# Kernel tuning notes

Measured on AMD Instinct MI355X. Metric: run time of the kernel, lower is better.

## Reference

```python
import jax, jax.numpy as jnp
import numpy as np

H = 512  # hidden size
E = 512  # embedding / input size
V = 10000  # vocab size


def _lstm_cell(x, h, c, W_ih, W_hh, b_ih, b_hh):
    # torch LSTMCell gate order: i, f, g, o
    gates = x @ W_ih.T + h @ W_hh.T + b_ih + b_hh
    i, f, g, o = jnp.split(gates, 4, axis=-1)
    i = jax.nn.sigmoid(i)
    f = jax.nn.sigmoid(f)
    g = jnp.tanh(g)
    o = jax.nn.sigmoid(o)
    c_new = f * c + i * g
    h_new = o * jnp.tanh(c_new)
    return h_new, c_new


def setup_inputs() -> dict:
    key = jax.random.key(0)
    ks = jax.random.split(key, 14)
    T, B, U = 128, 32, 1024
    s = 0.05
    return {
        "inputs": jax.random.normal(ks[0], (T, B, E), jnp.float32),
        "h0": jax.random.normal(ks[1], (2, B, H), jnp.float32),
        "c0": jax.random.normal(ks[2], (2, B, H), jnp.float32),
        "listener_outputs": jax.random.normal(ks[3], (U, B, H), jnp.float32),
        "W_ih1": jax.random.normal(ks[4], (4 * H, E), jnp.float32) * s,
        "W_hh1": jax.random.normal(ks[5], (4 * H, H), jnp.float32) * s,
        "b_ih1": jax.random.normal(ks[6], (4 * H,), jnp.float32) * s,
        "b_hh1": jax.random.normal(ks[7], (4 * H,), jnp.float32) * s,
        "W_ih2": jax.random.normal(ks[8], (4 * H, H), jnp.float32) * s,
        "W_hh2": jax.random.normal(ks[9], (4 * H, H), jnp.float32) * s,
        "b_ih2": jax.random.normal(ks[10], (4 * H,), jnp.float32) * s,
        "b_hh2": jax.random.normal(ks[11], (4 * H,), jnp.float32) * s,
        "W_out": jax.random.normal(ks[12], (V, H), jnp.float32) * s,
        "b_out": jax.random.normal(ks[13], (V,), jnp.float32) * s,
    }


def reference(inputs, h0, c0, listener_outputs,
              W_ih1, W_hh1, b_ih1, b_hh1,
              W_ih2, W_hh2, b_ih2, b_hh2,
              W_out, b_out):
    # layer-1 LSTMCell + dot-product attention per timestep
    def step1(carry, x_t):
        h1, c1 = carry
        h1, c1 = _lstm_cell(x_t, h1, c1, W_ih1, W_hh1, b_ih1, b_hh1)
        # scores over listener time U: (B, U)
        scores = jnp.einsum('ubh,bh->bu', listener_outputs, h1)
        w = jax.nn.softmax(scores, axis=1)
        ctx = jnp.einsum('ubh,bu->bh', listener_outputs, w)  # (B, H)
        return (h1, c1), ctx

    (_, _), contexts = jax.lax.scan(step1, (h0[0], c0[0]), inputs)  # (T, B, H)

    # layer-2 single-layer LSTM over attention contexts
    def step2(carry, x_t):
        h2, c2 = carry
        h2, c2 = _lstm_cell(x_t, h2, c2, W_ih2, W_hh2, b_ih2, b_hh2)
        return (h2, c2), h2

    (_, _), hs = jax.lax.scan(step2, (h0[1], c0[1]), contexts)  # (T, B, H)

    logits = hs @ W_out.T + b_out  # (T, B, V)
    return jax.nn.softmax(logits, axis=2)
```

## Files before the change

kernel.cpp:

```cpp
#include <hip/hip_runtime.h>

#define T_STEPS 128
#define BATCH   32
#define HID     512
#define EMB     512
#define ULEN    1024
#define VOCAB   10000
#define G4H     2048

#define ARR_STRIDE 16
#define GO_OFF     4096
#define GO_STRIDE  64
#define BAR_WORDS  6144

static inline int cdiv(int a, int b) { return (a + b - 1) / b; }

template <bool TRANSB>
__global__ __launch_bounds__(256)
void gemm_f32(const float* __restrict__ A, long lda, long sA,
              const float* __restrict__ Bm, long ldb, long sB,
              float* __restrict__ C, long ldc, long sC,
              int M, int N, int K, const float* __restrict__ bias)
{
    __shared__ float As[16][68];
    __shared__ float Bs[16][68];
    const int bz = blockIdx.z;
    A  += (size_t)bz * sA;
    Bm += (size_t)bz * sB;
    C  += (size_t)bz * sC;
    const int m0 = blockIdx.y * 64;
    const int n0 = blockIdx.x * 64;
    const int tid = threadIdx.x;
    const int tx = tid & 15, ty = tid >> 4;
    const int lr = tid >> 2;
    const int lk = (tid & 3) * 4;

    float acc[4][4] = {{0.f}};

    for (int k0 = 0; k0 < K; k0 += 16) {
        float4 av = *(const float4*)(A + (size_t)(m0 + lr) * lda + (k0 + lk));
        As[lk + 0][lr] = av.x; As[lk + 1][lr] = av.y;
        As[lk + 2][lr] = av.z; As[lk + 3][lr] = av.w;
        if (TRANSB) {
            const int nr = n0 + lr;
            float4 bv = make_float4(0.f, 0.f, 0.f, 0.f);
            if (nr < N) bv = *(const float4*)(Bm + (size_t)nr * ldb + (k0 + lk));
            Bs[lk + 0][lr] = bv.x; Bs[lk + 1][lr] = bv.y;
            Bs[lk + 2][lr] = bv.z; Bs[lk + 3][lr] = bv.w;
        } else {
            const int kr = tid >> 4;
            const int nc = (tid & 15) * 4;
            float4 bv = make_float4(0.f, 0.f, 0.f, 0.f);
            if (n0 + nc < N) bv = *(const float4*)(Bm + (size_t)(k0 + kr) * ldb + (n0 + nc));
            *(float4*)&Bs[kr][nc] = bv;
        }
        __syncthreads();
#pragma unroll
        for (int kk = 0; kk < 16; ++kk) {
            float ar[4], br[4];
#pragma unroll
            for (int i = 0; i < 4; i++) ar[i] = As[kk][ty * 4 + i];
#pragma unroll
            for (int j = 0; j < 4; j++) br[j] = Bs[kk][tx * 4 + j];
#pragma unroll
            for (int i = 0; i < 4; i++)
#pragma unroll
                for (int j = 0; j < 4; j++)
                    acc[i][j] += ar[i] * br[j];
        }
        __syncthreads();
    }
#pragma unroll
    for (int i = 0; i < 4; i++) {
        const int row = m0 + ty * 4 + i;
#pragma unroll
        for (int j = 0; j < 4; j++) {
            const int col = n0 + tx * 4 + j;
            if (col < N) {
                float v = acc[i][j];
                if (bias) v += bias[col];
                C[(size_t)row * ldc + col] = v;
            }
        }
    }
}

__device__ inline float sigmoidf_(float x) { return 1.f / (1.f + expf(-x)); }

__global__ __launch_bounds__(256, 1)
void lstm_scan(const float* __restrict__ gp,
               const float* __restrict__ Whh,
               const float* __restrict__ h0,
               const float* __restrict__ c0,
               float* __restrict__ h_all,
               unsigned* __restrict__ bar)
{
    __shared__ float h_lds[BATCH * HID];
    __shared__ float w_lds[8 * HID];
    __shared__ float part[256 * 36];
    unsigned* arrive = bar;

    const int tid  = threadIdx.x;
    const int bid  = blockIdx.x;
    const int hbase = bid * 2;

    const int ks = tid & 31;
    const int bq = tid >> 5;
    const int kl = ks & 7;

    const int b    = tid >> 3;
    const int nl   = tid & 7;
    const int j    = nl & 1;
    const int lane = tid & 63;
    const int sbase = lane & ~7;
    const int n = ((nl >> 1) << 9) + hbase + j;

#pragma unroll
    for (int i = 0; i < 4; ++i) {
        const int vi = i * 256 + tid;
        const int c  = vi >> 7;
        const int f  = vi & 127;
        const int nd = ((c >> 1) << 9) + hbase + (c & 1);
        float4 v = *(const float4*)(Whh + (size_t)nd * HID + f * 4);
        const int p = f ^ ((f >> 2) & 7);
        *(float4*)&w_lds[(c << 9) + (p << 2)] = v;
    }

    const int sw0 = (((ks * 4 + 0) ^ kl)) << 2;
    const int sw1 = (((ks * 4 + 1) ^ kl)) << 2;
    const int sw2 = (((ks * 4 + 2) ^ kl)) << 2;
    const int sw3 = (((ks * 4 + 3) ^ kl)) << 2;

    float c_state = (nl < 2) ? c0[b * HID + hbase + j] : 0.f;
    float gnext = gp[(size_t)b * G4H + n];

    for (int t = 0; t < T_STEPS; ++t) {
        float gval = gnext;

        const float* hsrc = (t == 0) ? h0 : (h_all + (size_t)(t - 1) * (BATCH * HID));
#pragma unroll
        for (int i = 0; i < 16; ++i) {
            const int vi = i * 256 + tid;
            float4 v = *(const float4*)(hsrc + (size_t)vi * 4);
            const int bb = vi >> 7;
            const int f  = vi & 127;
            const int p  = f ^ ((f >> 2) & 7);
            *(float4*)&h_lds[(bb << 9) + (p << 2)] = v;
        }
        __syncthreads();

        float4 hr[4][4];
#pragma unroll
        for (int rr = 0; rr < 4; ++rr) {
            const int o = (bq * 4 + rr) << 9;
            hr[rr][0] = *(const float4*)(h_lds + o + sw0);
            hr[rr][1] = *(const float4*)(h_lds + o + sw1);
            hr[rr][2] = *(const float4*)(h_lds + o + sw2);
            hr[rr][3] = *(const float4*)(h_lds + o + sw3);
        }

        float acc[32];
#pragma unroll
        for (int c = 0; c < 8; ++c) {
            const int wo = c << 9;
            float4 w0 = *(const float4*)(w_lds + wo + sw0);
            float4 w1 = *(const float4*)(w_lds + wo + sw1);
            float4 w2 = *(const float4*)(w_lds + wo + sw2);
            float4 w3 = *(const float4*)(w_lds + wo + sw3);
#pragma unroll
            for (int rr = 0; rr < 4; ++rr) {
                acc[rr * 8 + c] =
                      (hr[rr][0].x * w0.x + hr[rr][0].y * w0.y
                     + hr[rr][0].z * w0.z + hr[rr][0].w * w0.w)
                    + (hr[rr][1].x * w1.x + hr[rr][1].y * w1.y
                     + hr[rr][1].z * w1.z + hr[rr][1].w * w1.w)
                    + (hr[rr][2].x * w2.x + hr[rr][2].y * w2.y
                     + hr[rr][2].z * w2.z + hr[rr][2].w * w2.w)
                    + (hr[rr][3].x * w3.x + hr[rr][3].y * w3.y
                     + hr[rr][3].z * w3.z + hr[rr][3].w * w3.w);
            }
        }
        {
            float* pw = &part[tid * 36];
#pragma unroll
            for (int i = 0; i < 8; ++i)
                *(float4*)(pw + i * 4) =
                    make_float4(acc[4 * i], acc[4 * i + 1], acc[4 * i + 2], acc[4 * i + 3]);
        }
        __syncthreads();

        float s = gval;
        {
            const float* pr = &part[(b >> 2) * (32 * 36) + (b & 3) * 8 + nl];
#pragma unroll
            for (int kr = 0; kr < 32; ++kr) s += pr[kr * 36];
        }

        float fva = __shfl(s, sbase + 2 + j);
        float gva = __shfl(s, sbase + 4 + j);
        float ova = __shfl(s, sbase + 6 + j);
        if (nl < 2) {
            float iv = sigmoidf_(s);
            float fv = sigmoidf_(fva);
            float gv = tanhf(gva);
            float ov = sigmoidf_(ova);
            c_state = fv * c_state + iv * gv;
            float hn = ov * tanhf(c_state);
            __hip_atomic_store(h_all + ((size_t)t * BATCH + b) * HID + hbase + j,
                               hn, __ATOMIC_RELAXED, __HIP_MEMORY_SCOPE_AGENT);
        }

        {
            const int tn = (t + 1 < T_STEPS) ? (t + 1) : t;
            gnext = gp[((size_t)tn * BATCH + b) * G4H + n];
        }

        __syncthreads();
        const unsigned want = (unsigned)(t + 1);
        if (tid == 0)
            __hip_atomic_store(&arrive[bid * ARR_STRIDE], want, __ATOMIC_RELAXED,
                               __HIP_MEMORY_SCOPE_AGENT);
        if (tid < 64) {
            const unsigned* f0 = &arrive[(tid * 4 + 0) * ARR_STRIDE];
            const unsigned* f1 = &arrive[(tid * 4 + 1) * ARR_STRIDE];
            const unsigned* f2 = &arrive[(tid * 4 + 2) * ARR_STRIDE];
            const unsigned* f3 = &arrive[(tid * 4 + 3) * ARR_STRIDE];
            for (;;) {
                unsigned a = __hip_atomic_load(f0, __ATOMIC_RELAXED, __HIP_MEMORY_SCOPE_AGENT);
                unsigned b2 = __hip_atomic_load(f1, __ATOMIC_RELAXED, __HIP_MEMORY_SCOPE_AGENT);
                unsigned c2 = __hip_atomic_load(f2, __ATOMIC_RELAXED, __HIP_MEMORY_SCOPE_AGENT);
                unsigned d2 = __hip_atomic_load(f3, __ATOMIC_RELAXED, __HIP_MEMORY_SCOPE_AGENT);
                unsigned m0 = a < b2 ? a : b2;
                unsigned m1 = c2 < d2 ? c2 : d2;
                unsigned mn = m0 < m1 ? m0 : m1;
                if (__all(mn >= want)) break;
                __builtin_amdgcn_s_sleep(1);
            }
        }
        __syncthreads();
    }
}

__device__ inline float warpReduceMax_(float v) {
#pragma unroll
    for (int o = 32; o > 0; o >>= 1) v = fmaxf(v, __shfl_xor(v, o));
    return v;
}
__device__ inline float warpReduceSum_(float v) {
#pragma unroll
    for (int o = 32; o > 0; o >>= 1) v += __shfl_xor(v, o);
    return v;
}
__device__ inline float blockReduceMax_(float v, float* red) {
    v = warpReduceMax_(v);
    if ((threadIdx.x & 63) == 0) red[threadIdx.x >> 6] = v;
    __syncthreads();
    float r = fmaxf(fmaxf(red[0], red[1]), fmaxf(red[2], red[3]));
    __syncthreads();
    return r;
}
__device__ inline float blockReduceSum_(float v, float* red) {
    v = warpReduceSum_(v);
    if ((threadIdx.x & 63) == 0) red[threadIdx.x >> 6] = v;
    __syncthreads();
    float r = (red[0] + red[1]) + (red[2] + red[3]);
    __syncthreads();
    return r;
}

__global__ __launch_bounds__(256)
void softmax_u(float* __restrict__ s)
{
    __shared__ float red[4];
    float4* p = (float4*)(s + (size_t)blockIdx.x * ULEN);
    float4 v = p[threadIdx.x];
    float mx = fmaxf(fmaxf(v.x, v.y), fmaxf(v.z, v.w));
    mx = blockReduceMax_(mx, red);
    v.x = expf(v.x - mx); v.y = expf(v.y - mx);
    v.z = expf(v.z - mx); v.w = expf(v.w - mx);
    float sm = blockReduceSum_(v.x + v.y + v.z + v.w, red);
    float inv = 1.f / sm;
    v.x *= inv; v.y *= inv; v.z *= inv; v.w *= inv;
    p[threadIdx.x] = v;
}

__global__ __launch_bounds__(256)
void softmax_v(float* __restrict__ out)
{
    __shared__ float buf[VOCAB];
    __shared__ float red[4];
    float* p = out + (size_t)blockIdx.x * VOCAB;
    float mx = -INFINITY;
    for (int i = threadIdx.x; i < VOCAB; i += 256) {
        float x = p[i]; buf[i] = x; mx = fmaxf(mx, x);
    }
    mx = blockReduceMax_(mx, red);
    float sm = 0.f;
    for (int i = threadIdx.x; i < VOCAB; i += 256) {
        float e = expf(buf[i] - mx); buf[i] = e; sm += e;
    }
    sm = blockReduceSum_(sm, red);
    float inv = 1.f / sm;
    for (int i = threadIdx.x; i < VOCAB; i += 256) p[i] = buf[i] * inv;
}

__global__ void prep(const float* __restrict__ bi1, const float* __restrict__ bh1,
                     const float* __restrict__ bi2, const float* __restrict__ bh2,
                     float* __restrict__ bias1, float* __restrict__ bias2,
                     unsigned* __restrict__ flags)
{
    int i = blockIdx.x * 256 + threadIdx.x;
    if (i < G4H) { bias1[i] = bi1[i] + bh1[i]; bias2[i] = bi2[i] + bh2[i]; }
    if (i < 2 * BAR_WORDS) flags[i] = 0u;
}

extern "C" void kernel_launch(void* const* d_in, const int* in_sizes, int n_in,
                              void* d_out, int out_size, void* d_ws, size_t ws_size,
                              hipStream_t stream)
{
    const float* inputs = (const float*)d_in[0];
    const float* h0     = (const float*)d_in[1];
    const float* c0     = (const float*)d_in[2];
    const float* L      = (const float*)d_in[3];
    const float* W_ih1  = (const float*)d_in[4];
    const float* W_hh1  = (const float*)d_in[5];
    const float* b_ih1  = (const float*)d_in[6];
    const float* b_hh1  = (const float*)d_in[7];
    const float* W_ih2  = (const float*)d_in[8];
    const float* W_hh2  = (const float*)d_in[9];
    const float* b_ih2  = (const float*)d_in[10];
    const float* b_hh2  = (const float*)d_in[11];
    const float* W_out  = (const float*)d_in[12];
    const float* b_out  = (const float*)d_in[13];
    float* out = (float*)d_out;

    float* ws    = (float*)d_ws;
    float* gates = ws;
    float* h1    = gates + (size_t)T_STEPS * BATCH * G4H;
    float* h2    = h1    + (size_t)T_STEPS * BATCH * HID;
    float* ctx   = h2    + (size_t)T_STEPS * BATCH * HID;
    float* bias1 = ctx   + (size_t)T_STEPS * BATCH * HID;
    float* bias2 = bias1 + G4H;
    unsigned* flags = (unsigned*)(bias2 + G4H);
    float* scores = gates;

    prep<<<48, 256, 0, stream>>>(b_ih1, b_hh1, b_ih2, b_hh2, bias1, bias2, flags);

    gemm_f32<true><<<dim3(G4H / 64, (T_STEPS * BATCH) / 64, 1), 256, 0, stream>>>(
        inputs, EMB, 0, W_ih1, EMB, 0, gates, G4H, 0,
        T_STEPS * BATCH, G4H, EMB, bias1);

    lstm_scan<<<256, 256, 0, stream>>>(gates, W_hh1, h0, c0, h1, flags);

    gemm_f32<true><<<dim3(ULEN / 64, T_STEPS / 64, BATCH), 256, 0, stream>>>(
        h1, (long)BATCH * HID, HID,
        L,  (long)BATCH * HID, HID,
        scores, (long)BATCH * ULEN, ULEN,
        T_STEPS, ULEN, HID, nullptr);

    softmax_u<<<T_STEPS * BATCH, 256, 0, stream>>>(scores);

    gemm_f32<false><<<dim3(HID / 64, T_STEPS / 64, BATCH), 256, 0, stream>>>(
        scores, (long)BATCH * ULEN, ULEN,
        L,      (long)BATCH * HID,  HID,
        ctx,    (long)BATCH * HID,  HID,
        T_STEPS, HID, ULEN, nullptr);

    gemm_f32<true><<<dim3(G4H / 64, (T_STEPS * BATCH) / 64, 1), 256, 0, stream>>>(
        ctx, HID, 0, W_ih2, HID, 0, gates, G4H, 0,
        T_STEPS * BATCH, G4H, HID, bias2);

    lstm_scan<<<256, 256, 0, stream>>>(gates, W_hh2, h0 + BATCH * HID, c0 + BATCH * HID,
                                       h2, flags + BAR_WORDS);

    gemm_f32<true><<<dim3(cdiv(VOCAB, 64), (T_STEPS * BATCH) / 64, 1), 256, 0, stream>>>(
        h2, HID, 0, W_out, HID, 0, out, VOCAB, 0,
        T_STEPS * BATCH, VOCAB, HID, b_out);

    softmax_v<<<T_STEPS * BATCH, 256, 0, stream>>>(out);
}
```

Measured before the change: 2.680 ms.

## Enlarge GEMM tiles to 128x128 and centralize LSTM grid barrier via go flags

The fp32 GEMM moves from 64x64 tiles with a 4x4 per-thread micro-tile to 128x128 tiles with an 8x8 micro-tile (two 4x4 quadrants), vectorized LDS reads and float4 stores. This raises arithmetic intensity per LDS load. In exchange, fewer blocks run for the small batched attention GEMMs (T=128 gives a single row tile). Separately, the LSTM scan grid barrier becomes a master/worker scheme: block 0 gathers all arrival flags, then broadcasts through 32 go words that other blocks poll. This replaces every block polling all 256 flags, cutting polling traffic at the cost of an extra hop of latency per step.

Result: slower. 2.743 ms (+2.3%).

```diff
diff --git a/kernel.cpp b/kernel.cpp
--- a/kernel.cpp
+++ b/kernel.cpp
@@ -22,67 +22,100 @@
               float* __restrict__ C, long ldc, long sC,
               int M, int N, int K, const float* __restrict__ bias)
 {
-    __shared__ float As[16][68];
-    __shared__ float Bs[16][68];
+    __shared__ float As[8][128];
+    __shared__ float Bs[8][128];
     const int bz = blockIdx.z;
     A  += (size_t)bz * sA;
     Bm += (size_t)bz * sB;
     C  += (size_t)bz * sC;
-    const int m0 = blockIdx.y * 64;
-    const int n0 = blockIdx.x * 64;
+    const int m0 = blockIdx.y * 128;
+    const int n0 = blockIdx.x * 128;
     const int tid = threadIdx.x;
-    const int tx = tid & 15, ty = tid >> 4;
-    const int lr = tid >> 2;
-    const int lk = (tid & 3) * 4;
-
-    float acc[4][4] = {{0.f}};
-
-    for (int k0 = 0; k0 < K; k0 += 16) {
-        float4 av = *(const float4*)(A + (size_t)(m0 + lr) * lda + (k0 + lk));
-        As[lk + 0][lr] = av.x; As[lk + 1][lr] = av.y;
-        As[lk + 2][lr] = av.z; As[lk + 3][lr] = av.w;
+    const int tx = tid & 15;
+    const int ty = tid >> 4;
+    const int sr = tid >> 1;
+    const int sk = (tid & 1) * 4;
+
+    float acc[2][2][4][4];
+#pragma unroll
+    for (int ii = 0; ii < 2; ++ii)
+#pragma unroll
+        for (int jj = 0; jj < 2; ++jj)
+#pragma unroll
+            for (int i = 0; i < 4; ++i)
+#pragma unroll
+                for (int j = 0; j < 4; ++j) acc[ii][jj][i][j] = 0.f;
+
+    for (int k0 = 0; k0 < K; k0 += 8) {
+        {
+            float4 av = *(const float4*)(A + (size_t)(m0 + sr) * lda + (k0 + sk));
+            As[sk + 0][sr] = av.x; As[sk + 1][sr] = av.y;
+            As[sk + 2][sr] = av.z; As[sk + 3][sr] = av.w;
+        }
         if (TRANSB) {
-            const int nr = n0 + lr;
+            const int nr = n0 + sr;
             float4 bv = make_float4(0.f, 0.f, 0.f, 0.f);
-            if (nr < N) bv = *(const float4*)(Bm + (size_t)nr * ldb + (k0 + lk));
-            Bs[lk + 0][lr] = bv.x; Bs[lk + 1][lr] = bv.y;
-            Bs[lk + 2][lr] = bv.z; Bs[lk + 3][lr] = bv.w;
+            if (nr < N) bv = *(const float4*)(Bm + (size_t)nr * ldb + (k0 + sk));
+            Bs[sk + 0][sr] = bv.x; Bs[sk + 1][sr] = bv.y;
+            Bs[sk + 2][sr] = bv.z; Bs[sk + 3][sr] = bv.w;
         } else {
-            const int kr = tid >> 4;
-            const int nc = (tid & 15) * 4;
+            const int kr = tid >> 5;
+            const int ncc = (tid & 31) * 4;
             float4 bv = make_float4(0.f, 0.f, 0.f, 0.f);
-            if (n0 + nc < N) bv = *(const float4*)(Bm + (size_t)(k0 + kr) * ldb + (n0 + nc));
-            *(float4*)&Bs[kr][nc] = bv;
-        }
-        __syncthreads();
-#pragma unroll
-        for (int kk = 0; kk < 16; ++kk) {
-            float ar[4], br[4];
-#pragma unroll
-            for (int i = 0; i < 4; i++) ar[i] = As[kk][ty * 4 + i];
-#pragma unroll
-            for (int j = 0; j < 4; j++) br[j] = Bs[kk][tx * 4 + j];
-#pragma unroll
-            for (int i = 0; i < 4; i++)
-#pragma unroll
-                for (int j = 0; j < 4; j++)
-                    acc[i][j] += ar[i] * br[j];
+            if (n0 + ncc < N) bv = *(const float4*)(Bm + (size_t)(k0 + kr) * ldb + (n0 + ncc));
+            *(float4*)&Bs[kr][ncc] = bv;
+        }
+        __syncthreads();
+#pragma unroll
+        for (int kk = 0; kk < 8; ++kk) {
+            float4 a0 = *(const float4*)&As[kk][ty * 4];
+            float4 a1 = *(const float4*)&As[kk][64 + ty * 4];
+            float4 b0 = *(const float4*)&Bs[kk][tx * 4];
+            float4 b1 = *(const float4*)&Bs[kk][64 + tx * 4];
+            float ar[2][4] = {{a0.x, a0.y, a0.z, a0.w}, {a1.x, a1.y, a1.z, a1.w}};
+            float br[2][4] = {{b0.x, b0.y, b0.z, b0.w}, {b1.x, b1.y, b1.z, b1.w}};
+#pragma unroll
+            for (int ii = 0; ii < 2; ++ii)
+#pragma unroll
+                for (int jj = 0; jj < 2; ++jj)
+#pragma unroll
+                    for (int i = 0; i < 4; ++i)
+#pragma unroll
+                        for (int j = 0; j < 4; ++j)
+                            acc[ii][jj][i][j] += ar[ii][i] * br[jj][j];
         }
         __syncthreads();
     }
-#pragma unroll
-    for (int i = 0; i < 4; i++) {
-        const int row = m0 + ty * 4 + i;
-#pragma unroll
-        for (int j = 0; j < 4; j++) {
-            const int col = n0 + tx * 4 + j;
-            if (col < N) {
-                float v = acc[i][j];
-                if (bias) v += bias[col];
-                C[(size_t)row * ldc + col] = v;
+
+#pragma unroll
+    for (int ii = 0; ii < 2; ++ii)
+#pragma unroll
+        for (int i = 0; i < 4; ++i) {
+            const int row = m0 + ii * 64 + ty * 4 + i;
+#pragma unroll
+            for (int jj = 0; jj < 2; ++jj) {
+                const int cb = n0 + jj * 64 + tx * 4;
+                if (cb + 3 < N) {
+                    float4 v = make_float4(acc[ii][jj][i][0], acc[ii][jj][i][1],
+                                           acc[ii][jj][i][2], acc[ii][jj][i][3]);
+                    if (bias) {
+                        v.x += bias[cb + 0]; v.y += bias[cb + 1];
+                        v.z += bias[cb + 2]; v.w += bias[cb + 3];
+                    }
+                    *(float4*)(C + (size_t)row * ldc + cb) = v;
+                } else {
+#pragma unroll
+                    for (int j = 0; j < 4; ++j) {
+                        const int col = cb + j;
+                        if (col < N) {
+                            float v = acc[ii][jj][i][j];
+                            if (bias) v += bias[col];
+                            C[(size_t)row * ldc + col] = v;
+                        }
+                    }
+                }
             }
         }
-    }
 }
 
 __device__ inline float sigmoidf_(float x) { return 1.f / (1.f + expf(-x)); }
@@ -99,6 +132,7 @@
     __shared__ float w_lds[8 * HID];
     __shared__ float part[256 * 36];
     unsigned* arrive = bar;
+    unsigned* go     = bar + GO_OFF;
 
     const int tid  = threadIdx.x;
     const int bid  = blockIdx.x;
@@ -217,25 +251,27 @@
 
         __syncthreads();
         const unsigned want = (unsigned)(t + 1);
-        if (tid == 0)
+        if (bid == 0) {
+            if (tid == 0)
+                __hip_atomic_store(&arrive[0], want, __ATOMIC_RELAXED,
+                                   __HIP_MEMORY_SCOPE_AGENT);
+            unsigned v;
+            do {
+                v = __hip_atomic_load(&arrive[tid * ARR_STRIDE], __ATOMIC_RELAXED,
+                                      __HIP_MEMORY_SCOPE_AGENT);
+            } while (__syncthreads_count(v >= want) < 256);
+            if (tid < 32)
+                __hip_atomic_store(&go[tid * GO_STRIDE], want, __ATOMIC_RELAXED,
+                                   __HIP_MEMORY_SCOPE_AGENT);
+        } else if (tid == 0) {
             __hip_atomic_store(&arrive[bid * ARR_STRIDE], want, __ATOMIC_RELAXED,
                                __HIP_MEMORY_SCOPE_AGENT);
-        if (tid < 64) {
-            const unsigned* f0 = &arrive[(tid * 4 + 0) * ARR_STRIDE];
-            const unsigned* f1 = &arrive[(tid * 4 + 1) * ARR_STRIDE];
-            const unsigned* f2 = &arrive[(tid * 4 + 2) * ARR_STRIDE];
-            const unsigned* f3 = &arrive[(tid * 4 + 3) * ARR_STRIDE];
-            for (;;) {
-                unsigned a = __hip_atomic_load(f0, __ATOMIC_RELAXED, __HIP_MEMORY_SCOPE_AGENT);
-                unsigned b2 = __hip_atomic_load(f1, __ATOMIC_RELAXED, __HIP_MEMORY_SCOPE_AGENT);
-                unsigned c2 = __hip_atomic_load(f2, __ATOMIC_RELAXED, __HIP_MEMORY_SCOPE_AGENT);
-                unsigned d2 = __hip_atomic_load(f3, __ATOMIC_RELAXED, __HIP_MEMORY_SCOPE_AGENT);
-                unsigned m0 = a < b2 ? a : b2;
-                unsigned m1 = c2 < d2 ? c2 : d2;
-                unsigned mn = m0 < m1 ? m0 : m1;
-                if (__all(mn >= want)) break;
+            unsigned g;
+            do {
                 __builtin_amdgcn_s_sleep(1);
-            }
+                g = __hip_atomic_load(&go[(bid & 31) * GO_STRIDE], __ATOMIC_RELAXED,
+                                      __HIP_MEMORY_SCOPE_AGENT);
+            } while (g < want);
         }
         __syncthreads();
     }
@@ -346,13 +382,13 @@
 
     prep<<<48, 256, 0, stream>>>(b_ih1, b_hh1, b_ih2, b_hh2, bias1, bias2, flags);
 
-    gemm_f32<true><<<dim3(G4H / 64, (T_STEPS * BATCH) / 64, 1), 256, 0, stream>>>(
+    gemm_f32<true><<<dim3(G4H / 128, (T_STEPS * BATCH) / 128, 1), 256, 0, stream>>>(
         inputs, EMB, 0, W_ih1, EMB, 0, gates, G4H, 0,
         T_STEPS * BATCH, G4H, EMB, bias1);
 
     lstm_scan<<<256, 256, 0, stream>>>(gates, W_hh1, h0, c0, h1, flags);
 
-    gemm_f32<true><<<dim3(ULEN / 64, T_STEPS / 64, BATCH), 256, 0, stream>>>(
+    gemm_f32<true><<<dim3(ULEN / 128, T_STEPS / 128, BATCH), 256, 0, stream>>>(
         h1, (long)BATCH * HID, HID,
         L,  (long)BATCH * HID, HID,
         scores, (long)BATCH * ULEN, ULEN,
@@ -360,20 +396,20 @@
 
     softmax_u<<<T_STEPS * BATCH, 256, 0, stream>>>(scores);
 
-    gemm_f32<false><<<dim3(HID / 64, T_STEPS / 64, BATCH), 256, 0, stream>>>(
+    gemm_f32<false><<<dim3(HID / 128, T_STEPS / 128, BATCH), 256, 0, stream>>>(
         scores, (long)BATCH * ULEN, ULEN,
         L,      (long)BATCH * HID,  HID,
         ctx,    (long)BATCH * HID,  HID,
         T_STEPS, HID, ULEN, nullptr);
 
-    gemm_f32<true><<<dim3(G4H / 64, (T_STEPS * BATCH) / 64, 1), 256, 0, stream>>>(
+    gemm_f32<true><<<dim3(G4H / 128, (T_STEPS * BATCH) / 128, 1), 256, 0, stream>>>(
         ctx, HID, 0, W_ih2, HID, 0, gates, G4H, 0,
         T_STEPS * BATCH, G4H, HID, bias2);
 
     lstm_scan<<<256, 256, 0, stream>>>(gates, W_hh2, h0 + BATCH * HID, c0 + BATCH * HID,
                                        h2, flags + BAR_WORDS);
 
-    gemm_f32<true><<<dim3(cdiv(VOCAB, 64), (T_STEPS * BATCH) / 64, 1), 256, 0, stream>>>(
+    gemm_f32<true><<<dim3(cdiv(VOCAB, 128), (T_STEPS * BATCH) / 128, 1), 256, 0, stream>>>(
         h2, HID, 0, W_out, HID, 0, out, VOCAB, 0,
         T_STEPS * BATCH, VOCAB, HID, b_out);
 
```
